# Performance work log

Hardware: AMD Instinct MI355X
Metric: run time of the kernel (lower is better)

## Reference

```python
import jax, jax.numpy as jnp
import numpy as np
from jax.scipy.special import logsumexp

B, T, S, F = 16, 4096, 32, 64
LOG2PI = float(np.log(2.0 * np.pi))


def setup_inputs() -> dict:
    key = jax.random.key(0)
    k1, k2, k3, k4, k5 = jax.random.split(key, 5)
    x = jax.random.normal(k1, (B, T, F), dtype=jnp.float32)
    means = jax.random.normal(k2, (S, F), dtype=jnp.float32)
    # PSD full covariance per state: A A^T + I  (MultivariateNormal covariance_matrix)
    A = 0.1 * jax.random.normal(k3, (S, F, F), dtype=jnp.float32)
    covs = jnp.einsum('sfg,shg->sfh', A, A) + jnp.eye(F, dtype=jnp.float32)
    # Row-stochastic transition matrix and initial distribution, in log space.
    log_A = jax.nn.log_softmax(jax.random.normal(k4, (S, S), dtype=jnp.float32), axis=-1)
    log_pi = jax.nn.log_softmax(jax.random.normal(k5, (S,), dtype=jnp.float32))
    mask = jnp.ones((B, T), dtype=bool)
    return {'x': x, 'means': means, 'covs': covs, 'log_A': log_A, 'log_pi': log_pi, 'mask': mask}


def _emission_logprob(x, means, covs):
    # Multivariate Gaussian log pdf per (batch, time, state): logB[b,t,s]
    Fdim = x.shape[-1]
    P = jnp.linalg.inv(covs)                       # [S,F,F] precision
    logdet = jnp.linalg.slogdet(covs)[1]           # [S]
    diff = x[:, :, None, :] - means[None, None]    # [B,T,S,F]
    maha = jnp.einsum('btsf,sfg,btsg->bts', diff, P, diff)
    return -0.5 * (maha + Fdim * LOG2PI + logdet)


def _fb_single(logB, mask, log_A, log_pi):
    # Forward-backward DP for one sequence. logB: [T,S], mask: [T].
    neg_inf = jnp.array(-jnp.inf, logB.dtype)

    def fstep(a_prev, inp):
        lb, m = inp
        a = logsumexp(a_prev[:, None] + log_A, axis=0) + lb  # alpha[t,j]
        a = jnp.where(m, a, neg_inf)
        return a, a

    a0 = jnp.where(mask[0], log_pi + logB[0], neg_inf)
    _, alphas = jax.lax.scan(fstep, a0, (logB[1:], mask[1:]))
    alpha = jnp.concatenate([a0[None], alphas], axis=0)      # [T,S]

    def bstep(b_next, inp):
        lb_next, m_next = inp
        b = logsumexp(log_A + (lb_next + b_next)[None, :], axis=1)  # beta[t,j]
        b = jnp.where(m_next, b, b_next)  # freeze at 0 past the last valid frame
        return b, b

    bT = jnp.zeros(logB.shape[1], dtype=logB.dtype)
    _, betas = jax.lax.scan(bstep, bT, (logB[1:], mask[1:]), reverse=True)
    beta = jnp.concatenate([betas, bT[None]], axis=0)        # [T,S]
    beta = jnp.where(mask[:, None], beta, neg_inf)
    return alpha, beta


def reference(x, means, covs, log_A, log_pi, mask):
    logB = _emission_logprob(x, means, covs)                  # [B,T,S]
    alpha, beta = jax.vmap(_fb_single, in_axes=(0, 0, None, None))(logB, mask, log_A, log_pi)
    lengths = mask.sum(axis=-1)                               # [B]
    idx = jnp.broadcast_to((lengths - 1)[:, None, None], (alpha.shape[0], 1, alpha.shape[2]))
    alpha_last = jnp.take_along_axis(alpha, idx, axis=1)[:, 0, :]
    evidence = logsumexp(alpha_last, axis=-1)                 # [B] log p(x_{1:l})
    gamma = alpha + beta - evidence[:, None, None]            # log posterior state marginals
    return gamma
```

## Files before the change

### kernel.cpp

```cpp
#include <hip/hip_runtime.h>
#include <math.h>

#define Tt 4096
#define NB 16

#define CLN2PI 1.8378770664093453f

#define OFF_W    0
#define OFF_D    131072
#define OFF_CST  133120
#define OFF_EV   133152
#define OFF_LB   133184
#define OFF_BET  2230336

__device__ __forceinline__ float rdlane(float x, int l) {
  return __int_as_float(__builtin_amdgcn_readlane(__float_as_int(x), l));
}

__global__ __launch_bounds__(64) void k_chol(const float* __restrict__ covs,
                                             const float* __restrict__ means,
                                             float* __restrict__ ws) {
  __shared__ float Am[64][65];
  __shared__ float Wl[64][65];
  int s = blockIdx.x, j = threadIdx.x;
  for (int r = 0; r < 64; ++r) {
    Am[r][j] = covs[((size_t)s * 64 + r) * 64 + j];
    Wl[r][j] = 0.f;
  }
  __syncthreads();
  for (int k = 0; k < 64; ++k) {
    float diag = sqrtf(Am[k][k]);
    float col = (j > k) ? Am[j][k] / diag : 0.f;
    __syncthreads();
    if (j == k) Am[k][k] = diag;
    if (j > k)  Am[j][k] = col;
    __syncthreads();
    if (j > k) {
      for (int g = k + 1; g <= j; ++g) Am[j][g] -= col * Am[g][k];
    }
    __syncthreads();
  }
  {
    int c = j;
    Wl[c][c] = 1.0f / Am[c][c];
    for (int f = c + 1; f < 64; ++f) {
      float ssum = 0.f;
      for (int g = c; g < f; ++g) ssum += Am[f][g] * Wl[g][c];
      Wl[f][c] = -ssum / Am[f][f];
    }
  }
  __syncthreads();
  for (int r = 0; r < 64; ++r)
    ws[OFF_W + ((size_t)s * 64 + r) * 64 + j] = Wl[r][j];
  {
    float acc = 0.f;
    for (int g = 0; g < 64; ++g) acc += Wl[j][g] * means[s * 64 + g];
    ws[OFF_D + s * 64 + j] = acc;
  }
  if (j == 0) {
    float logdet = 0.f;
    for (int k = 0; k < 64; ++k) logdet += __logf(Am[k][k]);
    logdet *= 2.0f;
    ws[OFF_CST + s] = 64.0f * CLN2PI + logdet;
  }
}

__global__ __launch_bounds__(64) void k_emis(const float* __restrict__ x,
                                             const float* __restrict__ wsr,
                                             float* __restrict__ lb) {
  const float* W = wsr + OFF_W;
  const float* D = wsr + OFF_D;
  const float* C = wsr + OFF_CST;
  int bx = blockIdx.x;
  int sgrp = bx & 3;
  int pt = (bx >> 2) * 64 + threadIdx.x;
  const float* xr = x + (size_t)pt * 64;
  float xv[64];
#pragma unroll
  for (int c = 0; c < 16; ++c) {
    float4 q = ((const float4*)xr)[c];
    xv[4 * c + 0] = q.x; xv[4 * c + 1] = q.y;
    xv[4 * c + 2] = q.z; xv[4 * c + 3] = q.w;
  }
#pragma unroll 1
  for (int si = 0; si < 8; ++si) {
    int s = sgrp * 8 + si;
    const float* Ws = W + (size_t)s * 4096;
    const float* Ds = D + s * 64;
    float maha = 0.f;
#pragma unroll
    for (int f = 0; f < 64; ++f) {
      float z = -Ds[f];
#pragma unroll
      for (int ch = 0; ch < 4; ++ch) {
        if (ch <= (f >> 4)) {
#pragma unroll
          for (int gg = 0; gg < 16; ++gg) {
            int g = ch * 16 + gg;
            z = fmaf(Ws[f * 64 + g], xv[g], z);
          }
        }
      }
      maha = fmaf(z, z, maha);
    }
    lb[(size_t)pt * 32 + s] = -0.5f * (maha + C[s]);
  }
}

__device__ __forceinline__ float npsum32(const float* z) {
  float r[8];
#pragma unroll
  for (int k = 0; k < 8; ++k)
    r[k] = ((z[k] + z[k + 8]) + z[k + 16]) + z[k + 24];
  return ((r[0] + r[1]) + (r[2] + r[3])) + ((r[4] + r[5]) + (r[6] + r[7]));
}
__device__ __forceinline__ float max32(const float* z) {
  float t16[16];
#pragma unroll
  for (int k = 0; k < 16; ++k) t16[k] = fmaxf(z[k], z[k + 16]);
  float t8[8];
#pragma unroll
  for (int k = 0; k < 8; ++k) t8[k] = fmaxf(t16[k], t16[k + 8]);
  float t4[4];
#pragma unroll
  for (int k = 0; k < 4; ++k) t4[k] = fmaxf(t8[k], t8[k + 4]);
  float t2a = fmaxf(t4[0], t4[2]), t2b = fmaxf(t4[1], t4[3]);
  return fmaxf(t2a, t2b);
}

__global__ __launch_bounds__(64, 1) __attribute__((amdgpu_waves_per_eu(1)))
void k_fb(const float* __restrict__ logA,
          const float* __restrict__ logpi,
          float* __restrict__ ws,
          float* __restrict__ out) {
  const float* lbg = ws + OFF_LB;
  float* bet = ws + OFF_BET;
  float* ev  = ws + OFF_EV;
  int chain = blockIdx.x;
  int b   = chain & 15;
  int dir = chain >> 4;
  int lane = threadIdx.x;
  int j = lane & 31;
  const float* lb = lbg + (size_t)b * Tt * 32;
  float z[32];
  if (dir == 0) {
    float acol[32];
#pragma unroll
    for (int i = 0; i < 32; ++i) {
      acol[i] = logA[i * 32 + j];
      asm volatile("" : "+v"(acol[i]));
    }
    float* ao = out + (size_t)b * Tt * 32;
    float a = logpi[j] + lb[j];
    ao[j] = a;
    float bA = lb[32 + j];
    float bB = lb[64 + j];
    float bC = lb[96 + j];
#pragma unroll 1
    for (int t = 1; t < Tt; ++t) {
      float bcur = bA; bA = bB; bB = bC;
      if (t + 3 < Tt) bC = lb[(size_t)(t + 3) * 32 + j];
#pragma unroll
      for (int i = 0; i < 32; ++i) z[i] = rdlane(a, i) + acol[i];
      float m = max32(z);
#pragma unroll
      for (int i = 0; i < 32; ++i) z[i] = __expf(z[i] - m);
      float S = npsum32(z);
      a = (__logf(S) + m) + bcur;
      ao[(size_t)t * 32 + j] = a;
    }
#pragma unroll
    for (int i = 0; i < 32; ++i) z[i] = rdlane(a, i);
    float m = max32(z);
#pragma unroll
    for (int i = 0; i < 32; ++i) z[i] = __expf(z[i] - m);
    float S = npsum32(z);
    if (lane == 0) ev[b] = __logf(S) + m;
  } else {
    float arow[32];
#pragma unroll
    for (int i = 0; i < 32; ++i) {
      arow[i] = logA[j * 32 + i];
      asm volatile("" : "+v"(arow[i]));
    }
    float* bo = bet + (size_t)b * Tt * 32;
    bo[(size_t)(Tt - 1) * 32 + j] = 0.f;
    float y = lb[(size_t)(Tt - 1) * 32 + j] + 0.f;
    float bA = lb[(size_t)(Tt - 2) * 32 + j];
    float bB = lb[(size_t)(Tt - 3) * 32 + j];
    float bC = lb[(size_t)(Tt - 4) * 32 + j];
#pragma unroll 1
    for (int t = Tt - 2; t >= 0; --t) {
      float bcur = bA; bA = bB; bB = bC;
      if (t >= 3) bC = lb[(size_t)(t - 3) * 32 + j];
#pragma unroll
      for (int i = 0; i < 32; ++i) z[i] = arow[i] + rdlane(y, i);
      float m = max32(z);
#pragma unroll
      for (int i = 0; i < 32; ++i) z[i] = __expf(z[i] - m);
      float S = npsum32(z);
      float bv = __logf(S) + m;
      bo[(size_t)t * 32 + j] = bv;
      y = bcur + bv;
    }
  }
}

__global__ void k_gamma(const float* __restrict__ ws, float* __restrict__ out) {
  size_t idx = (size_t)blockIdx.x * blockDim.x + threadIdx.x;
  if (idx >= (size_t)NB * Tt * 32) return;
  int b = (int)(idx >> 17);
  float a  = out[idx];
  float bb = ws[OFF_BET + idx];
  float e  = ws[OFF_EV + b];
  out[idx] = (a + bb) - e;
}

extern "C" void kernel_launch(void* const* d_in, const int* in_sizes, int n_in,
                              void* d_out, int out_size, void* d_ws, size_t ws_size,
                              hipStream_t stream) {
  const float* x     = (const float*)d_in[0];
  const float* means = (const float*)d_in[1];
  const float* covs  = (const float*)d_in[2];
  const float* logA  = (const float*)d_in[3];
  const float* logpi = (const float*)d_in[4];
  float* ws  = (float*)d_ws;
  float* out = (float*)d_out;

  k_chol<<<dim3(32), dim3(64), 0, stream>>>(covs, means, ws);
  k_emis<<<dim3(4096), dim3(64), 0, stream>>>(x, ws, ws + OFF_LB);
  k_fb<<<dim3(32), dim3(64), 0, stream>>>(logA, logpi, ws, out);
  k_gamma<<<dim3(8192), dim3(256), 0, stream>>>(ws, out);
}
```

Baseline: 2.492 ms.

## Split forward-backward logsumexp across both wave halves using ds_bpermute

The forward and backward recursions now use all 64 lanes. Each half-wave handles 16 of the 32 source states and reads them with ds_bpermute instead of 32 readlanes. Partial maxima and sums are exchanged between the halves with bpermute, and the upper half's result is broadcast back so both halves hold the same state. This halves the per-lane exp and add work on the serial critical path. In exchange it adds LDS-crossbar permute latency (several dependent bpermutes per step) on a latency-bound loop.

```diff
diff --git a/kernel.cpp b/kernel.cpp
--- a/kernel.cpp
+++ b/kernel.cpp
@@ -15,6 +15,9 @@
 
 __device__ __forceinline__ float rdlane(float x, int l) {
   return __int_as_float(__builtin_amdgcn_readlane(__float_as_int(x), l));
+}
+__device__ __forceinline__ float bpmf(int addr, float x) {
+  return __int_as_float(__builtin_amdgcn_ds_bpermute(addr, __float_as_int(x)));
 }
 
 __global__ __launch_bounds__(64) void k_chol(const float* __restrict__ covs,
@@ -126,6 +129,15 @@
   for (int k = 0; k < 4; ++k) t4[k] = fmaxf(t8[k], t8[k + 4]);
   float t2a = fmaxf(t4[0], t4[2]), t2b = fmaxf(t4[1], t4[3]);
   return fmaxf(t2a, t2b);
+}
+__device__ __forceinline__ float max16(const float* z) {
+  float t8[8];
+#pragma unroll
+  for (int k = 0; k < 8; ++k) t8[k] = fmaxf(z[k], z[k + 8]);
+  float t4[4];
+#pragma unroll
+  for (int k = 0; k < 4; ++k) t4[k] = fmaxf(t8[k], t8[k + 4]);
+  return fmaxf(fmaxf(t4[0], t4[2]), fmaxf(t4[1], t4[3]));
 }
 
 __global__ __launch_bounds__(64, 1) __attribute__((amdgpu_waves_per_eu(1)))
@@ -141,14 +153,25 @@
   int dir = chain >> 4;
   int lane = threadIdx.x;
   int j = lane & 31;
+  int h = lane >> 5;
+  int i0 = h << 4;
+  int xaddr = (lane ^ 32) << 2;
+  int baddr = (lane | 32) << 2;
   const float* lb = lbg + (size_t)b * Tt * 32;
-  float z[32];
+
+  int gaddr[16];
+#pragma unroll
+  for (int k = 0; k < 16; ++k) {
+    gaddr[k] = (i0 + k) << 2;
+    asm volatile("" : "+v"(gaddr[k]));
+  }
+
   if (dir == 0) {
-    float acol[32];
-#pragma unroll
-    for (int i = 0; i < 32; ++i) {
-      acol[i] = logA[i * 32 + j];
-      asm volatile("" : "+v"(acol[i]));
+    float acol[16];
+#pragma unroll
+    for (int k = 0; k < 16; ++k) {
+      acol[k] = logA[(i0 + k) * 32 + j];
+      asm volatile("" : "+v"(acol[k]));
     }
     float* ao = out + (size_t)b * Tt * 32;
     float a = logpi[j] + lb[j];
@@ -160,15 +183,27 @@
     for (int t = 1; t < Tt; ++t) {
       float bcur = bA; bA = bB; bB = bC;
       if (t + 3 < Tt) bC = lb[(size_t)(t + 3) * 32 + j];
-#pragma unroll
-      for (int i = 0; i < 32; ++i) z[i] = rdlane(a, i) + acol[i];
-      float m = max32(z);
-#pragma unroll
-      for (int i = 0; i < 32; ++i) z[i] = __expf(z[i] - m);
-      float S = npsum32(z);
-      a = (__logf(S) + m) + bcur;
+      float z[16];
+#pragma unroll
+      for (int k = 0; k < 16; ++k) z[k] = bpmf(gaddr[k], a) + acol[k];
+      float mh = max16(z);
+      float m = fmaxf(mh, bpmf(xaddr, mh));
+      float e[16];
+#pragma unroll
+      for (int k = 0; k < 16; ++k) e[k] = __expf(z[k] - m);
+      float p[8];
+#pragma unroll
+      for (int k = 0; k < 8; ++k) p[k] = e[k] + e[k + 8];
+      float r[8];
+#pragma unroll
+      for (int k = 0; k < 8; ++k)
+        r[k] = (bpmf(xaddr, p[k]) + e[k]) + e[k + 8];
+      float S = ((r[0] + r[1]) + (r[2] + r[3])) + ((r[4] + r[5]) + (r[6] + r[7]));
+      float anew = (__logf(S) + m) + bcur;
+      a = bpmf(baddr, anew);
       ao[(size_t)t * 32 + j] = a;
     }
+    float z[32];
 #pragma unroll
     for (int i = 0; i < 32; ++i) z[i] = rdlane(a, i);
     float m = max32(z);
@@ -177,11 +212,11 @@
     float S = npsum32(z);
     if (lane == 0) ev[b] = __logf(S) + m;
   } else {
-    float arow[32];
-#pragma unroll
-    for (int i = 0; i < 32; ++i) {
-      arow[i] = logA[j * 32 + i];
-      asm volatile("" : "+v"(arow[i]));
+    float arow[16];
+#pragma unroll
+    for (int k = 0; k < 16; ++k) {
+      arow[k] = logA[j * 32 + i0 + k];
+      asm volatile("" : "+v"(arow[k]));
     }
     float* bo = bet + (size_t)b * Tt * 32;
     bo[(size_t)(Tt - 1) * 32 + j] = 0.f;
@@ -193,13 +228,24 @@
     for (int t = Tt - 2; t >= 0; --t) {
       float bcur = bA; bA = bB; bB = bC;
       if (t >= 3) bC = lb[(size_t)(t - 3) * 32 + j];
-#pragma unroll
-      for (int i = 0; i < 32; ++i) z[i] = arow[i] + rdlane(y, i);
-      float m = max32(z);
-#pragma unroll
-      for (int i = 0; i < 32; ++i) z[i] = __expf(z[i] - m);
-      float S = npsum32(z);
-      float bv = __logf(S) + m;
+      float z[16];
+#pragma unroll
+      for (int k = 0; k < 16; ++k) z[k] = arow[k] + bpmf(gaddr[k], y);
+      float mh = max16(z);
+      float m = fmaxf(mh, bpmf(xaddr, mh));
+      float e[16];
+#pragma unroll
+      for (int k = 0; k < 16; ++k) e[k] = __expf(z[k] - m);
+      float p[8];
+#pragma unroll
+      for (int k = 0; k < 8; ++k) p[k] = e[k] + e[k + 8];
+      float r[8];
+#pragma unroll
+      for (int k = 0; k < 8; ++k)
+        r[k] = (bpmf(xaddr, p[k]) + e[k]) + e[k + 8];
+      float S = ((r[0] + r[1]) + (r[2] + r[3])) + ((r[4] + r[5]) + (r[6] + r[7]));
+      float bvu = __logf(S) + m;
+      float bv = bpmf(baddr, bvu);
       bo[(size_t)t * 32 + j] = bv;
       y = bcur + bv;
     }
```

Result: no change. 2.466 ms (-1.1%).

## Split forward-backward logsumexp across two waves with LDS partial merge

Applied to the files above, without the earlier changes.

Each forward/backward chain now runs on two wavefronts. Each 32-lane half of each wave handles 8 of the 32 source states, and the halves are combined with permlane32_swap. Per-wave (max, sum) partials are then exchanged through double-buffered LDS with a barrier every time step. This shortens the per-step serial dependency chain of 32 exps and reductions, but adds a workgroup barrier and an LDS round trip on every one of the 4096 steps.

```diff
diff --git a/kernel.cpp b/kernel.cpp
--- a/kernel.cpp
+++ b/kernel.cpp
@@ -15,6 +15,14 @@
 
 __device__ __forceinline__ float rdlane(float x, int l) {
   return __int_as_float(__builtin_amdgcn_readlane(__float_as_int(x), l));
+}
+
+typedef unsigned int u32x2 __attribute__((ext_vector_type(2)));
+__device__ __forceinline__ void xhalf(float v, float& lo, float& hi) {
+  u32x2 r = __builtin_amdgcn_permlane32_swap(__float_as_uint(v), __float_as_uint(v),
+                                             false, false);
+  lo = __uint_as_float(r.x);
+  hi = __uint_as_float(r.y);
 }
 
 __global__ __launch_bounds__(64) void k_chol(const float* __restrict__ covs,
@@ -127,32 +135,49 @@
   float t2a = fmaxf(t4[0], t4[2]), t2b = fmaxf(t4[1], t4[3]);
   return fmaxf(t2a, t2b);
 }
-
-__global__ __launch_bounds__(64, 1) __attribute__((amdgpu_waves_per_eu(1)))
+__device__ __forceinline__ float max8(const float* z) {
+  float t4[4];
+#pragma unroll
+  for (int k = 0; k < 4; ++k) t4[k] = fmaxf(z[k], z[k + 4]);
+  return fmaxf(fmaxf(t4[0], t4[2]), fmaxf(t4[1], t4[3]));
+}
+__device__ __forceinline__ float sum8(const float* e) {
+  float t4[4];
+#pragma unroll
+  for (int k = 0; k < 4; ++k) t4[k] = e[k] + e[k + 4];
+  return (t4[0] + t4[2]) + (t4[1] + t4[3]);
+}
+
+__global__ __launch_bounds__(128, 1) __attribute__((amdgpu_waves_per_eu(1)))
 void k_fb(const float* __restrict__ logA,
           const float* __restrict__ logpi,
           float* __restrict__ ws,
           float* __restrict__ out) {
+  __shared__ float2 partsMS[2][2][2][32];
   const float* lbg = ws + OFF_LB;
   float* bet = ws + OFF_BET;
   float* ev  = ws + OFF_EV;
   int chain = blockIdx.x;
   int b   = chain & 15;
   int dir = chain >> 4;
-  int lane = threadIdx.x;
+  int tid = threadIdx.x;
+  int w   = tid >> 6;
+  int lane = tid & 63;
+  int q = lane >> 5;
   int j = lane & 31;
+  int ib = (w << 4) + (q << 3);
   const float* lb = lbg + (size_t)b * Tt * 32;
-  float z[32];
+
   if (dir == 0) {
-    float acol[32];
-#pragma unroll
-    for (int i = 0; i < 32; ++i) {
-      acol[i] = logA[i * 32 + j];
-      asm volatile("" : "+v"(acol[i]));
+    float ac[8];
+#pragma unroll
+    for (int k = 0; k < 8; ++k) {
+      ac[k] = logA[(ib + k) * 32 + j];
+      asm volatile("" : "+v"(ac[k]));
     }
     float* ao = out + (size_t)b * Tt * 32;
     float a = logpi[j] + lb[j];
-    ao[j] = a;
+    if (w == 0) ao[j] = a;
     float bA = lb[32 + j];
     float bB = lb[64 + j];
     float bC = lb[96 + j];
@@ -160,31 +185,61 @@
     for (int t = 1; t < Tt; ++t) {
       float bcur = bA; bA = bB; bB = bC;
       if (t + 3 < Tt) bC = lb[(size_t)(t + 3) * 32 + j];
-#pragma unroll
-      for (int i = 0; i < 32; ++i) z[i] = rdlane(a, i) + acol[i];
+      float sa[16];
+#pragma unroll
+      for (int k = 0; k < 16; ++k) sa[k] = rdlane(a, 16 * w + k);
+      float z[8];
+      if (q == 0) {
+#pragma unroll
+        for (int k = 0; k < 8; ++k) z[k] = sa[k] + ac[k];
+      } else {
+#pragma unroll
+        for (int k = 0; k < 8; ++k) z[k] = sa[8 + k] + ac[k];
+      }
+      float mq = max8(z);
+      float mlo, mhi; xhalf(mq, mlo, mhi);
+      float mw = fmaxf(mlo, mhi);
+      float e[8];
+#pragma unroll
+      for (int k = 0; k < 8; ++k) e[k] = __expf(z[k] - mw);
+      float sq = sum8(e);
+      float slo, shi; xhalf(sq, slo, shi);
+      float Sw = slo + shi;
+      int p = t & 1;
+      partsMS[p][w][q][j] = make_float2(mw, Sw);
+      asm volatile("s_waitcnt lgkmcnt(0)" ::: "memory");
+      __builtin_amdgcn_s_barrier();
+      asm volatile("" ::: "memory");
+      float2 oth = partsMS[p][w ^ 1][0][j];
+      float mo = oth.x, So = oth.y;
+      float m = fmaxf(mw, mo);
+      float m0 = (w == 0) ? mw : mo;
+      float S0 = (w == 0) ? Sw : So;
+      float m1 = (w == 0) ? mo : mw;
+      float S1 = (w == 0) ? So : Sw;
+      float S = S0 * __expf(m0 - m) + S1 * __expf(m1 - m);
+      a = (__logf(S) + m) + bcur;
+      if (w == 0) ao[(size_t)t * 32 + j] = a;
+    }
+    if (w == 0) {
+      float z[32];
+#pragma unroll
+      for (int i = 0; i < 32; ++i) z[i] = rdlane(a, i);
       float m = max32(z);
 #pragma unroll
       for (int i = 0; i < 32; ++i) z[i] = __expf(z[i] - m);
       float S = npsum32(z);
-      a = (__logf(S) + m) + bcur;
-      ao[(size_t)t * 32 + j] = a;
-    }
-#pragma unroll
-    for (int i = 0; i < 32; ++i) z[i] = rdlane(a, i);
-    float m = max32(z);
-#pragma unroll
-    for (int i = 0; i < 32; ++i) z[i] = __expf(z[i] - m);
-    float S = npsum32(z);
-    if (lane == 0) ev[b] = __logf(S) + m;
+      if (lane == 0) ev[b] = __logf(S) + m;
+    }
   } else {
-    float arow[32];
-#pragma unroll
-    for (int i = 0; i < 32; ++i) {
-      arow[i] = logA[j * 32 + i];
-      asm volatile("" : "+v"(arow[i]));
+    float ar[8];
+#pragma unroll
+    for (int k = 0; k < 8; ++k) {
+      ar[k] = logA[j * 32 + ib + k];
+      asm volatile("" : "+v"(ar[k]));
     }
     float* bo = bet + (size_t)b * Tt * 32;
-    bo[(size_t)(Tt - 1) * 32 + j] = 0.f;
+    if (w == 0) bo[(size_t)(Tt - 1) * 32 + j] = 0.f;
     float y = lb[(size_t)(Tt - 1) * 32 + j] + 0.f;
     float bA = lb[(size_t)(Tt - 2) * 32 + j];
     float bB = lb[(size_t)(Tt - 3) * 32 + j];
@@ -193,14 +248,41 @@
     for (int t = Tt - 2; t >= 0; --t) {
       float bcur = bA; bA = bB; bB = bC;
       if (t >= 3) bC = lb[(size_t)(t - 3) * 32 + j];
-#pragma unroll
-      for (int i = 0; i < 32; ++i) z[i] = arow[i] + rdlane(y, i);
-      float m = max32(z);
-#pragma unroll
-      for (int i = 0; i < 32; ++i) z[i] = __expf(z[i] - m);
-      float S = npsum32(z);
+      float sy[16];
+#pragma unroll
+      for (int k = 0; k < 16; ++k) sy[k] = rdlane(y, 16 * w + k);
+      float z[8];
+      if (q == 0) {
+#pragma unroll
+        for (int k = 0; k < 8; ++k) z[k] = ar[k] + sy[k];
+      } else {
+#pragma unroll
+        for (int k = 0; k < 8; ++k) z[k] = ar[k] + sy[8 + k];
+      }
+      float mq = max8(z);
+      float mlo, mhi; xhalf(mq, mlo, mhi);
+      float mw = fmaxf(mlo, mhi);
+      float e[8];
+#pragma unroll
+      for (int k = 0; k < 8; ++k) e[k] = __expf(z[k] - mw);
+      float sq = sum8(e);
+      float slo, shi; xhalf(sq, slo, shi);
+      float Sw = slo + shi;
+      int p = t & 1;
+      partsMS[p][w][q][j] = make_float2(mw, Sw);
+      asm volatile("s_waitcnt lgkmcnt(0)" ::: "memory");
+      __builtin_amdgcn_s_barrier();
+      asm volatile("" ::: "memory");
+      float2 oth = partsMS[p][w ^ 1][0][j];
+      float mo = oth.x, So = oth.y;
+      float m = fmaxf(mw, mo);
+      float m0 = (w == 0) ? mw : mo;
+      float S0 = (w == 0) ? Sw : So;
+      float m1 = (w == 0) ? mo : mw;
+      float S1 = (w == 0) ? So : Sw;
+      float S = S0 * __expf(m0 - m) + S1 * __expf(m1 - m);
       float bv = __logf(S) + m;
-      bo[(size_t)t * 32 + j] = bv;
+      if (w == 0) bo[(size_t)t * 32 + j] = bv;
       y = bcur + bv;
     }
   }
@@ -229,6 +311,6 @@
 
   k_chol<<<dim3(32), dim3(64), 0, stream>>>(covs, means, ws);
   k_emis<<<dim3(4096), dim3(64), 0, stream>>>(x, ws, ws + OFF_LB);
-  k_fb<<<dim3(32), dim3(64), 0, stream>>>(logA, logpi, ws, out);
+  k_fb<<<dim3(32), dim3(128), 0, stream>>>(logA, logpi, ws, out);
   k_gamma<<<dim3(8192), dim3(256), 0, stream>>>(ws, out);
 }
```

New measurement: 2.834 ms. 1.14x slower.
